# Performance work log

Measured on AMD Instinct MI355X. Metric: run time of the kernel, lower is better.

## Reference

```python
import jax, jax.numpy as jnp
import numpy as np

EPS_BN = 1e-3  # nn.BatchNorm1d(num_channels, eps=0.001)
B, C, N = 16, 256, 2048
NUM_SA = 4


def _bn(x, g, b, m, v):
    # eval-mode BatchNorm1d over channel dim of [B, C, N]
    return g[:, None] * (x - m[:, None]) * jax.lax.rsqrt(v[:, None] + EPS_BN) + b[:, None]


def _sa_layer(x, qk_w, v_w, v_b, t_w, t_b, g, b, m, var):
    # q_conv and k_conv share weights -> energy = (Wx)^T (Wx)
    q = jnp.einsum('oc,bcn->bon', qk_w, x)              # [B, C//4, N]
    energy = jnp.einsum('bcm,bcn->bmn', q, q)           # [B, N, N]
    attn = jax.nn.softmax(energy, axis=-1)
    # offset-attention: extra column-sum normalization (dim=1)
    attn = attn / (1e-9 + attn.sum(axis=1, keepdims=True))
    xv = jnp.einsum('oc,bcn->bon', v_w, x) + v_b[:, None]   # [B, C, N]
    x_r = jnp.einsum('bcn,bnm->bcm', xv, attn)              # bmm(x_v, attention)
    t = jnp.einsum('oc,bcn->bon', t_w, x - x_r) + t_b[:, None]
    return x + jax.nn.relu(_bn(t, g, b, m, var))


def setup_inputs() -> dict:
    key = jax.random.key(0)
    ks = jax.random.split(key, 24)
    f32 = jnp.float32
    d = {}
    d['x'] = jax.random.normal(ks[0], (B, C, N), dtype=f32)
    d['conv1_w'] = jax.random.normal(ks[1], (C, C), dtype=f32) * 0.05
    d['conv2_w'] = jax.random.normal(ks[2], (C, C), dtype=f32) * 0.05
    for i, nm in enumerate(['bn1', 'bn2']):
        kk = jax.random.split(ks[3 + i], 4)
        d[nm + '_g'] = 1.0 + 0.05 * jax.random.normal(kk[0], (C,), dtype=f32)
        d[nm + '_b'] = 0.05 * jax.random.normal(kk[1], (C,), dtype=f32)
        d[nm + '_m'] = 0.05 * jax.random.normal(kk[2], (C,), dtype=f32)
        d[nm + '_v'] = jax.random.uniform(kk[3], (C,), dtype=f32, minval=0.5, maxval=1.5)
    d['sa_qk_w'] = jax.random.normal(ks[5], (NUM_SA, C // 4, C), dtype=f32) * 0.05
    d['sa_v_w'] = jax.random.normal(ks[6], (NUM_SA, C, C), dtype=f32) * 0.05
    d['sa_v_b'] = jax.random.normal(ks[7], (NUM_SA, C), dtype=f32) * 0.05
    d['sa_t_w'] = jax.random.normal(ks[8], (NUM_SA, C, C), dtype=f32) * 0.05
    d['sa_t_b'] = jax.random.normal(ks[9], (NUM_SA, C), dtype=f32) * 0.05
    d['sa_g'] = 1.0 + 0.05 * jax.random.normal(ks[10], (NUM_SA, C), dtype=f32)
    d['sa_b'] = 0.05 * jax.random.normal(ks[11], (NUM_SA, C), dtype=f32)
    d['sa_m'] = 0.05 * jax.random.normal(ks[12], (NUM_SA, C), dtype=f32)
    d['sa_var'] = jax.random.uniform(ks[13], (NUM_SA, C), dtype=f32, minval=0.5, maxval=1.5)
    d['flag'] = 0  # False -> primary bn branch
    return d


def reference(x, conv1_w, conv2_w, bn1_g, bn1_b, bn1_m, bn1_v,
              bn2_g, bn2_b, bn2_m, bn2_v,
              sa_qk_w, sa_v_w, sa_v_b, sa_t_w, sa_t_b,
              sa_g, sa_b, sa_m, sa_var, flag):
    h = jax.nn.relu(_bn(jnp.einsum('oc,bcn->bon', conv1_w, x), bn1_g, bn1_b, bn1_m, bn1_v))
    h = jax.nn.relu(_bn(jnp.einsum('oc,bcn->bon', conv2_w, h), bn2_g, bn2_b, bn2_m, bn2_v))
    outs = []
    for i in range(NUM_SA):
        h = _sa_layer(h, sa_qk_w[i], sa_v_w[i], sa_v_b[i], sa_t_w[i], sa_t_b[i],
                      sa_g[i], sa_b[i], sa_m[i], sa_var[i])
        outs.append(h)
    return jnp.concatenate(outs, axis=1)  # [B, 4*C, N]
```

## Files before the change

### kernel.cpp

```cpp
#include <hip/hip_runtime.h>
#include <hip/hip_bf16.h>
#include <hip/hip_fp16.h>

static constexpr int Bn = 16;
static constexpr int Cc = 256;
static constexpr int Nn = 2048;
static constexpr int C4 = 64;
static constexpr float LOG2E = 1.4426950408889634f;

typedef _Float16 half_t;
typedef __attribute__((ext_vector_type(8))) _Float16 half8;
typedef __attribute__((ext_vector_type(4))) _Float16 half4;
typedef __attribute__((ext_vector_type(8))) short short8;
typedef __attribute__((ext_vector_type(4))) float float4v;

static constexpr long sNC = (long)Nn * Cc;
static constexpr long sNQ = (long)Nn * C4;

#define DEVI __device__ __forceinline__

DEVI float bf2f(unsigned short u) { return __uint_as_float(((unsigned)u) << 16); }
DEVI unsigned short f2bf(float f) {
    unsigned x = __float_as_uint(f);
    x += 0x7fffu + ((x >> 16) & 1u);
    return (unsigned short)(x >> 16);
}

DEVI void gload16(const void* g, void* l) {
    __builtin_amdgcn_global_load_lds(
        (const __attribute__((address_space(1))) unsigned int*)g,
        (__attribute__((address_space(3))) unsigned int*)l, 16, 0, 0);
}

enum { EPI_RAW = 0, EPI_H = 1, EPI_XV = 2, EPI_T = 4 };

template<int MODE, int BM, int BN, int WI, int WJ, bool BF16OUT>
__global__ __launch_bounds__(256)
void mgemm(const half_t* __restrict__ A, long aB,
           const half_t* __restrict__ Bm, long bB,
           void* __restrict__ Yv, long yB, int ldy,
           const half_t* __restrict__ Haux, long hB,
           half_t* __restrict__ hNext, long hnB,
           const float* __restrict__ bias,
           const float* __restrict__ bng, const float* __restrict__ bnb,
           const float* __restrict__ bnm, const float* __restrict__ bnv,
           int K)
{
    __shared__ __align__(16) half_t Als[2][BM][32];
    __shared__ __align__(16) half_t Bls[2][BN][32];

    const int tid  = threadIdx.x;
    const int w    = tid >> 6;
    const int lane = tid & 63;
    const int wi   = (WI == 1) ? 0 : (w & (WI - 1));
    const int wj   = (WI == 1) ? w : (w >> 1);
    const int quad = lane >> 4, m16 = lane & 15;
    const int lr   = lane >> 2, lc = lane & 3;
    const int b    = blockIdx.z;
    const int j0   = blockIdx.x * BN;
    const int i0   = blockIdx.y * BM;

    const half_t* Ab = A + (size_t)b * aB;
    const half_t* Bb = Bm + (size_t)b * bB;

    float4v acc[4][4];
    #pragma unroll
    for (int i = 0; i < 4; ++i)
        #pragma unroll
        for (int j = 0; j < 4; ++j) acc[i][j] = (float4v)0.f;

    for (int k0 = 0; k0 < K; k0 += 64) {
        #pragma unroll
        for (int s = 0; s < 2; ++s) {
            const int kk = k0 + s * 32 + lc * 8;
            #pragma unroll
            for (int t = 0; t < BM / 64; ++t) {
                const int row = (t * 4 + w) * 16;
                gload16(Ab + (size_t)(i0 + row + lr) * K + kk, &Als[s][row][0]);
            }
            #pragma unroll
            for (int t = 0; t < BN / 64; ++t) {
                const int row = (t * 4 + w) * 16;
                gload16(Bb + (size_t)(j0 + row + lr) * K + kk, &Bls[s][row][0]);
            }
        }
        __syncthreads();
        #pragma unroll
        for (int s = 0; s < 2; ++s) {
            half8 af[4], bf[4];
            #pragma unroll
            for (int t = 0; t < 4; ++t)
                af[t] = *(const half8*)&Als[s][wi * 64 + t * 16 + m16][quad * 8];
            #pragma unroll
            for (int t = 0; t < 4; ++t)
                bf[t] = *(const half8*)&Bls[s][wj * 64 + t * 16 + m16][quad * 8];
            #pragma unroll
            for (int ti = 0; ti < 4; ++ti)
                #pragma unroll
                for (int tj = 0; tj < 4; ++tj)
                    acc[ti][tj] = __builtin_amdgcn_mfma_f32_16x16x32_f16(
                        af[ti], bf[tj], acc[ti][tj], 0, 0, 0);
        }
        __syncthreads();
    }

    #pragma unroll
    for (int ti = 0; ti < 4; ++ti) {
        const int il = i0 + wi * 64 + ti * 16 + quad * 4;
        #pragma unroll
        for (int tj = 0; tj < 4; ++tj) {
            const int jl = j0 + wj * 64 + tj * 16 + m16;
            float4v v = acc[ti][tj];
            if (MODE == EPI_RAW) {
                half4 o;
                #pragma unroll
                for (int r = 0; r < 4; ++r) o[r] = (half_t)v[r];
                *(half4*)((half_t*)Yv + (size_t)b * yB + (size_t)jl * ldy + il) = o;
            } else if (MODE == EPI_H) {
                half4 o;
                #pragma unroll
                for (int r = 0; r < 4; ++r) {
                    const float sc = bng[il + r] * rsqrtf(bnv[il + r] + 1e-3f);
                    const float sh = bnb[il + r] - bnm[il + r] * sc;
                    o[r] = (half_t)fmaxf(fmaf(v[r], sc, sh), 0.f);
                }
                *(half4*)((half_t*)Yv + (size_t)b * yB + (size_t)jl * ldy + il) = o;
            } else if (MODE == EPI_XV) {
                const float bj = bias[jl];
                if (BF16OUT) {
                    ushort4 o;
                    o.x = f2bf(v[0] + bj); o.y = f2bf(v[1] + bj);
                    o.z = f2bf(v[2] + bj); o.w = f2bf(v[3] + bj);
                    *(ushort4*)((unsigned short*)Yv + (size_t)b * yB + (size_t)jl * ldy + il) = o;
                } else {
                    half4 o;
                    #pragma unroll
                    for (int r = 0; r < 4; ++r) o[r] = (half_t)(v[r] + bj);
                    *(half4*)((half_t*)Yv + (size_t)b * yB + (size_t)jl * ldy + il) = o;
                }
            } else {
                const float tb2 = bias[jl];
                const float sc  = bng[jl] * rsqrtf(bnv[jl] + 1e-3f);
                const float sh  = bnb[jl] - bnm[jl] * sc;
                float4v o;
                #pragma unroll
                for (int r = 0; r < 4; ++r) {
                    const float t2  = v[r] + tb2;
                    const float rel = fmaxf(fmaf(t2, sc, sh), 0.f);
                    const float hv  = (float)Haux[(size_t)b * hB + (size_t)(il + r) * Cc + jl];
                    const float ov  = hv + rel;
                    o[r] = ov;
                    if (hNext)
                        hNext[(size_t)b * hnB + (size_t)(il + r) * Cc + jl] = (half_t)ov;
                }
                *(float4v*)((float*)Yv + (size_t)b * yB + (size_t)jl * ldy + il) = o;
            }
        }
    }
}

__global__ __launch_bounds__(256)
void estats(const half_t* __restrict__ q, float* __restrict__ Pbuf)
{
    __shared__ __align__(16) half_t sA[128 * 64];
    __shared__ __align__(16) half_t sB[128 * 64];
    __shared__ float red[2][2][4][16][2];
    const int tid = threadIdx.x, w = tid >> 6, lane = tid & 63;
    const int wi = w & 1, wj = w >> 1, quad = lane >> 4, m16 = lane & 15;
    const int b = blockIdx.z, j0 = blockIdx.x * 128, i0 = blockIdx.y * 128;
    const half_t* qb = q + (size_t)b * sNQ;

    #pragma unroll
    for (int t = 0; t < 4; ++t) {
        const int g = w * 256 + t * 64 + lane;
        const int r = g >> 3, c = g & 7;
        const int cs = c ^ (r & 7);
        gload16(qb + (size_t)(i0 + r) * 64 + cs * 8, sA + (w * 256 + t * 64) * 8);
        gload16(qb + (size_t)(j0 + r) * 64 + cs * 8, sB + (w * 256 + t * 64) * 8);
    }
    __syncthreads();

    half8 an[4][2], bm[4][2];
    #pragma unroll
    for (int t = 0; t < 4; ++t)
        #pragma unroll
        for (int ks = 0; ks < 2; ++ks) {
            const int pc = ((ks * 4 + quad) ^ (m16 & 7)) * 8;
            an[t][ks] = *(const half8*)&sA[(wi * 64 + t * 16 + m16) * 64 + pc];
            bm[t][ks] = *(const half8*)&sB[(wj * 64 + t * 16 + m16) * 64 + pc];
        }

    #pragma unroll
    for (int tj = 0; tj < 4; ++tj) {
        float4v e[4];
        #pragma unroll
        for (int ti = 0; ti < 4; ++ti) {
            e[ti] = (float4v)0.f;
            e[ti] = __builtin_amdgcn_mfma_f32_16x16x32_f16(an[ti][0], bm[tj][0], e[ti], 0, 0, 0);
            e[ti] = __builtin_amdgcn_mfma_f32_16x16x32_f16(an[ti][1], bm[tj][1], e[ti], 0, 0, 0);
        }
        float lmax = -1e30f;
        #pragma unroll
        for (int ti = 0; ti < 4; ++ti)
            #pragma unroll
            for (int r = 0; r < 4; ++r) lmax = fmaxf(lmax, e[ti][r]);
        lmax = fmaxf(lmax, __shfl_xor(lmax, 16));
        lmax = fmaxf(lmax, __shfl_xor(lmax, 32));
        float ls = 0.f;
        #pragma unroll
        for (int ti = 0; ti < 4; ++ti)
            #pragma unroll
            for (int r = 0; r < 4; ++r) ls += __expf(e[ti][r] - lmax);
        ls += __shfl_xor(ls, 16);
        ls += __shfl_xor(ls, 32);
        if (quad == 0) { red[wi][wj][tj][m16][0] = lmax; red[wi][wj][tj][m16][1] = ls; }
    }
    __syncthreads();
    if (tid < 128) {
        const int wj2 = tid >> 6, tj2 = (tid >> 4) & 3, mm = tid & 15;
        const float m0 = red[0][wj2][tj2][mm][0], s0 = red[0][wj2][tj2][mm][1];
        const float m1 = red[1][wj2][tj2][mm][0], s1 = red[1][wj2][tj2][mm][1];
        const float M = fmaxf(m0, m1);
        const float S = s0 * __expf(m0 - M) + s1 * __expf(m1 - M);
        const int m = j0 + wj2 * 64 + tj2 * 16 + mm;
        *(float2*)(Pbuf + (((size_t)b * Nn + m) * 16 + blockIdx.y) * 2) = make_float2(M, S);
    }
}

__global__ __launch_bounds__(256)
void statsreduce(const float* __restrict__ Pbuf, float* __restrict__ off)
{
    const int id = blockIdx.x * 256 + threadIdx.x;
    const int b = id >> 11, m = id & 2047;
    const float2* p = (const float2*)(Pbuf + ((size_t)b * Nn + m) * 32);
    float M = -1e30f;
    #pragma unroll
    for (int i = 0; i < 16; ++i) M = fmaxf(M, p[i].x);
    float S = 0.f;
    #pragma unroll
    for (int i = 0; i < 16; ++i) S += p[i].y * __expf(p[i].x - M);
    off[(size_t)b * Nn + m] = fmaf(M, LOG2E, __log2f(S));
}

__global__ __launch_bounds__(512, 4)
void flashxr(const half_t* __restrict__ q, const half_t* __restrict__ xv,
             const half_t* __restrict__ h, const float* __restrict__ off,
             half_t* __restrict__ dS)
{
    __shared__ __align__(16) half_t sQ[128 * 64];
    __shared__ __align__(16) half_t sXV[128 * 128];
    __shared__ __align__(16) half_t sP[128 * 128];

    const int tid = threadIdx.x, w = tid >> 6, lane = tid & 63;
    const int wi = w & 1, wj = w >> 1, quad = lane >> 4, m16 = lane & 15;
    const int b = blockIdx.z, j0 = blockIdx.x * 128, i0 = blockIdx.y * 128;
    const half_t* qb  = q + (size_t)b * sNQ;
    const half_t* xvb = xv + (size_t)b * sNC;

    #pragma unroll
    for (int t = 0; t < 2; ++t) {
        const int g = w * 128 + t * 64 + lane;
        const int r = g >> 3, c = g & 7;
        gload16(qb + (size_t)(j0 + r) * 64 + (c ^ (r & 7)) * 8, sP + (w * 128 + t * 64) * 8);
    }
    __syncthreads();
    half8 bq[2][2];
    #pragma unroll
    for (int tj = 0; tj < 2; ++tj)
        #pragma unroll
        for (int ks = 0; ks < 2; ++ks)
            bq[tj][ks] = *(const half8*)&sP[(wj * 32 + tj * 16 + m16) * 64
                                            + (((ks * 4 + quad) ^ (m16 & 7)) * 8)];
    __syncthreads();

    float4v acc[4][2];
    #pragma unroll
    for (int i = 0; i < 4; ++i)
        #pragma unroll
        for (int j = 0; j < 2; ++j) acc[i][j] = (float4v)0.f;
    float csa[2] = {0.f, 0.f};

    const float* offb = off + (size_t)b * Nn;

    for (int nc = 0; nc < 16; ++nc) {
        #pragma unroll
        for (int t = 0; t < 2; ++t) {
            const int g = w * 128 + t * 64 + lane;
            const int r = g >> 3, c = g & 7;
            gload16(qb + (size_t)(nc * 128 + r) * 64 + (c ^ (r & 7)) * 8,
                    sQ + (w * 128 + t * 64) * 8);
        }
        #pragma unroll
        for (int t = 0; t < 4; ++t) {
            const int g = w * 256 + t * 64 + lane;
            const int r = g >> 4, c = g & 15;
            gload16(xvb + (size_t)(i0 + r) * Nn + nc * 128 + (c ^ (r & 15)) * 8,
                    sXV + (w * 256 + t * 64) * 8);
        }
        __syncthreads();

        const int nbase = nc * 128 + wi * 64 + quad * 4;
        #pragma unroll
        for (int ti = 0; ti < 4; ++ti) {
            const int arow = (wi * 64 + ti * 16 + m16) * 64;
            const half8 an0 = *(const half8*)&sQ[arow + ((quad ^ (m16 & 7)) * 8)];
            const half8 an1 = *(const half8*)&sQ[arow + (((4 + quad) ^ (m16 & 7)) * 8)];
            float4v e0 = (float4v)0.f, e1 = (float4v)0.f;
            e0 = __builtin_amdgcn_mfma_f32_16x16x32_f16(an0, bq[0][0], e0, 0, 0, 0);
            e1 = __builtin_amdgcn_mfma_f32_16x16x32_f16(an0, bq[1][0], e1, 0, 0, 0);
            e0 = __builtin_amdgcn_mfma_f32_16x16x32_f16(an1, bq[0][1], e0, 0, 0, 0);
            e1 = __builtin_amdgcn_mfma_f32_16x16x32_f16(an1, bq[1][1], e1, 0, 0, 0);
            const float4v o4 = *(const float4v*)&offb[nbase + ti * 16];
            const int pc = wi * 8 + ti * 2 + (quad >> 1);
            const int sub = (quad & 1) * 4;
            {
                float c0 = 0.f; ushort4 pk;
                #pragma unroll
                for (int r = 0; r < 4; ++r) {
                    const float p = __builtin_amdgcn_exp2f(fmaf(e0[r], LOG2E, -o4[r]));
                    c0 += p; (&pk.x)[r] = f2bf(p);
                }
                csa[0] += c0;
                const int mrow = wj * 32 + m16;
                *(ushort4*)&((unsigned short*)sP)[(size_t)mrow * 128 + (pc ^ m16) * 8 + sub] = pk;
            }
            {
                float c1 = 0.f; ushort4 pk;
                #pragma unroll
                for (int r = 0; r < 4; ++r) {
                    const float p = __builtin_amdgcn_exp2f(fmaf(e1[r], LOG2E, -o4[r]));
                    c1 += p; (&pk.x)[r] = f2bf(p);
                }
                csa[1] += c1;
                const int mrow = wj * 32 + 16 + m16;
                *(ushort4*)&((unsigned short*)sP)[(size_t)mrow * 128 + (pc ^ m16) * 8 + sub] = pk;
            }
        }
        __syncthreads();

        #pragma unroll
        for (int ks = 0; ks < 4; ++ks) {
            short8 xa[4], pb[2];
            #pragma unroll
            for (int ti = 0; ti < 4; ++ti)
                xa[ti] = *(const short8*)&sXV[(wi * 64 + ti * 16 + m16) * 128
                                              + (((ks * 4 + quad) ^ m16) * 8)];
            #pragma unroll
            for (int tj = 0; tj < 2; ++tj)
                pb[tj] = *(const short8*)&sP[(wj * 32 + tj * 16 + m16) * 128
                                             + (((ks * 4 + quad) ^ m16) * 8)];
            #pragma unroll
            for (int ti = 0; ti < 4; ++ti)
                #pragma unroll
                for (int tj = 0; tj < 2; ++tj)
                    acc[ti][tj] = __builtin_amdgcn_mfma_f32_16x16x32_bf16(
                        xa[ti], pb[tj], acc[ti][tj], 0, 0, 0);
        }
        __syncthreads();
    }

    #pragma unroll
    for (int tj = 0; tj < 2; ++tj) {
        csa[tj] += __shfl_xor(csa[tj], 16);
        csa[tj] += __shfl_xor(csa[tj], 32);
    }
    float* fb = (float*)sP;
    if (lane < 16) {
        #pragma unroll
        for (int tj = 0; tj < 2; ++tj)
            fb[wi * 128 + wj * 32 + tj * 16 + lane] = csa[tj];
    }
    __syncthreads();
    float csr[2];
    #pragma unroll
    for (int tj = 0; tj < 2; ++tj) {
        const float c0 = fb[0   + wj * 32 + tj * 16 + m16];
        const float c1 = fb[128 + wj * 32 + tj * 16 + m16];
        csr[tj] = 1.0f / (1e-9f + c0 + c1);
    }

    const half_t* hb = h + (size_t)b * sNC;
    half_t* db = dS + (size_t)b * sNC;
    #pragma unroll
    for (int ti = 0; ti < 4; ++ti) {
        const int cg = i0 + wi * 64 + ti * 16 + quad * 4;
        #pragma unroll
        for (int tj = 0; tj < 2; ++tj) {
            const int mg = j0 + wj * 32 + tj * 16 + m16;
            const half4 hv = *(const half4*)&hb[(size_t)mg * Cc + cg];
            half4 o;
            #pragma unroll
            for (int r = 0; r < 4; ++r)
                o[r] = (half_t)((float)hv[r] - acc[ti][tj][r] * csr[tj]);
            *(half4*)&db[(size_t)mg * Cc + cg] = o;
        }
    }
}

__global__ __launch_bounds__(256)
void xpose_cast(const float* __restrict__ x, half_t* __restrict__ xT)
{
    __shared__ half_t tile[32][33];
    const int tx = threadIdx.x & 31, ty = threadIdx.x >> 5;
    const int n0 = blockIdx.x * 32, c0 = blockIdx.y * 32, b = blockIdx.z;
    #pragma unroll
    for (int r = 0; r < 4; ++r)
        tile[ty * 4 + r][tx] =
            (half_t)x[((size_t)b * Cc + c0 + ty * 4 + r) * Nn + n0 + tx];
    __syncthreads();
    #pragma unroll
    for (int r = 0; r < 4; ++r)
        xT[((size_t)b * Nn + n0 + ty * 4 + r) * Cc + c0 + tx] = tile[tx][ty * 4 + r];
}

__global__ __launch_bounds__(256)
void castall(const float* __restrict__ c1, const float* __restrict__ c2,
             const float* __restrict__ qk, const float* __restrict__ vw,
             const float* __restrict__ tw, half_t* __restrict__ dst)
{
    const int i = (blockIdx.x * 256 + threadIdx.x) * 4;
    const float* s; int o;
    if      (i < 65536)  { s = c1; o = 0; }
    else if (i < 131072) { s = c2; o = 65536; }
    else if (i < 196608) { s = qk; o = 131072; }
    else if (i < 458752) { s = vw; o = 196608; }
    else                 { s = tw; o = 458752; }
    const float4v v = *(const float4v*)(s + (i - o));
    half4 out;
    #pragma unroll
    for (int r = 0; r < 4; ++r) out[r] = (half_t)v[r];
    *(half4*)(dst + i) = out;
}

extern "C" void kernel_launch(void* const* d_in, const int* in_sizes, int n_in,
                              void* d_out, int out_size, void* d_ws, size_t ws_size,
                              hipStream_t stream)
{
    const float* x    = (const float*)d_in[0];
    const float* c1w  = (const float*)d_in[1];
    const float* c2w  = (const float*)d_in[2];
    const float* bn1g = (const float*)d_in[3], *bn1b = (const float*)d_in[4];
    const float* bn1m = (const float*)d_in[5], *bn1v = (const float*)d_in[6];
    const float* bn2g = (const float*)d_in[7], *bn2b = (const float*)d_in[8];
    const float* bn2m = (const float*)d_in[9], *bn2v = (const float*)d_in[10];
    const float* qkw  = (const float*)d_in[11];
    const float* vw   = (const float*)d_in[12];
    const float* vb   = (const float*)d_in[13];
    const float* tw   = (const float*)d_in[14];
    const float* tb   = (const float*)d_in[15];
    const float* sag  = (const float*)d_in[16];
    const float* sab  = (const float*)d_in[17];
    const float* sam  = (const float*)d_in[18];
    const float* sav  = (const float*)d_in[19];
    float* out = (float*)d_out;

    char* ws = (char*)d_ws;
    const size_t HSZ = (size_t)Bn * Nn * Cc * 2;
    half_t* xT   = (half_t*)(ws);
    half_t* hA   = (half_t*)(ws + HSZ);
    half_t* hBuf = (half_t*)(ws + 2 * HSZ);
    half_t* q_s  = (half_t*)(ws + 3 * HSZ);
    half_t* xv_s = (half_t*)(ws + 3 * HSZ + (size_t)4194304);
    half_t* d_s  = (half_t*)(ws + 4 * HSZ + (size_t)4194304);
    float*  offp = (float*) (ws + 5 * HSZ + (size_t)4194304);
    float*  Pbuf = (float*) (ws + 5 * HSZ + (size_t)4325376);
    half_t* warena = (half_t*)(ws + 5 * HSZ + (size_t)8519680);
    half_t* wc1  = warena;
    half_t* wc2  = wc1 + 65536;
    half_t* wqk  = wc2 + 65536;
    half_t* wv   = wqk + 65536;
    half_t* wt   = wv  + 262144;

    dim3 blk(256);

    castall<<<768, blk, 0, stream>>>(c1w, c2w, qkw, vw, tw, warena);
    xpose_cast<<<dim3(Nn / 32, Cc / 32, Bn), blk, 0, stream>>>(x, xT);

    mgemm<EPI_H, 128, 128, 2, 2, false><<<dim3(16, 2, Bn), blk, 0, stream>>>(
        wc1, 0, xT, sNC, hA, sNC, Cc, nullptr, 0, nullptr, 0,
        nullptr, bn1g, bn1b, bn1m, bn1v, Cc);
    mgemm<EPI_H, 128, 128, 2, 2, false><<<dim3(16, 2, Bn), blk, 0, stream>>>(
        wc2, 0, hA, sNC, hBuf, sNC, Cc, nullptr, 0, nullptr, 0,
        nullptr, bn2g, bn2b, bn2m, bn2v, Cc);

    half_t* hcur = hBuf;
    half_t* hnxt = hA;
    for (int L = 0; L < 4; ++L) {
        mgemm<EPI_RAW, 64, 256, 1, 4, false><<<dim3(8, 1, Bn), blk, 0, stream>>>(
            wqk + (long)L * C4 * Cc, 0, hcur, sNC, q_s, sNQ, C4,
            nullptr, 0, nullptr, 0,
            nullptr, nullptr, nullptr, nullptr, nullptr, Cc);
        estats<<<dim3(16, 16, Bn), blk, 0, stream>>>(q_s, Pbuf);
        statsreduce<<<128, blk, 0, stream>>>(Pbuf, offp);
        mgemm<EPI_XV, 128, 128, 2, 2, true><<<dim3(2, 16, Bn), blk, 0, stream>>>(
            hcur, sNC, wv + (long)L * Cc * Cc, 0, xv_s, (long)Cc * Nn, Nn,
            nullptr, 0, nullptr, 0,
            vb + L * Cc, nullptr, nullptr, nullptr, nullptr, Cc);
        flashxr<<<dim3(16, 2, Bn), dim3(512), 0, stream>>>(
            q_s, xv_s, hcur, offp, d_s);
        mgemm<EPI_T, 128, 128, 2, 2, false><<<dim3(2, 16, Bn), blk, 0, stream>>>(
            d_s, sNC, wt + (long)L * Cc * Cc, 0,
            out + (long)L * Cc * Nn, (long)4 * Cc * Nn, Nn,
            hcur, sNC, (L < 3) ? hnxt : nullptr, sNC,
            tb + L * Cc, sag + L * Cc, sab + L * Cc, sam + L * Cc, sav + L * Cc,
            Cc);
        half_t* tmp = hcur; hcur = hnxt; hnxt = tmp;
    }
}
```

Baseline: 806.9 us.

## Widen flash kernel to full channel tile and enlarge GEMM blocks to 512 threads

```diff
diff --git a/kernel.cpp b/kernel.cpp
--- a/kernel.cpp
+++ b/kernel.cpp
@@ -35,7 +35,7 @@
 enum { EPI_RAW = 0, EPI_H = 1, EPI_XV = 2, EPI_T = 4 };
 
 template<int MODE, int BM, int BN, int WI, int WJ, bool BF16OUT>
-__global__ __launch_bounds__(256)
+__global__ __launch_bounds__(WI * WJ * 64)
 void mgemm(const half_t* __restrict__ A, long aB,
            const half_t* __restrict__ Bm, long bB,
            void* __restrict__ Yv, long yB, int ldy,
@@ -46,14 +46,15 @@
            const float* __restrict__ bnm, const float* __restrict__ bnv,
            int K)
 {
+    constexpr int NW = WI * WJ;
     __shared__ __align__(16) half_t Als[2][BM][32];
     __shared__ __align__(16) half_t Bls[2][BN][32];
 
     const int tid  = threadIdx.x;
     const int w    = tid >> 6;
     const int lane = tid & 63;
-    const int wi   = (WI == 1) ? 0 : (w & (WI - 1));
-    const int wj   = (WI == 1) ? w : (w >> 1);
+    const int wi   = w % WI;
+    const int wj   = w / WI;
     const int quad = lane >> 4, m16 = lane & 15;
     const int lr   = lane >> 2, lc = lane & 3;
     const int b    = blockIdx.z;
@@ -74,13 +75,13 @@
         for (int s = 0; s < 2; ++s) {
             const int kk = k0 + s * 32 + lc * 8;
             #pragma unroll
-            for (int t = 0; t < BM / 64; ++t) {
-                const int row = (t * 4 + w) * 16;
+            for (int t = 0; t < BM / (16 * NW); ++t) {
+                const int row = (t * NW + w) * 16;
                 gload16(Ab + (size_t)(i0 + row + lr) * K + kk, &Als[s][row][0]);
             }
             #pragma unroll
-            for (int t = 0; t < BN / 64; ++t) {
-                const int row = (t * 4 + w) * 16;
+            for (int t = 0; t < BN / (16 * NW); ++t) {
+                const int row = (t * NW + w) * 16;
                 gload16(Bb + (size_t)(j0 + row + lr) * K + kk, &Bls[s][row][0]);
             }
         }
@@ -242,35 +243,34 @@
     off[(size_t)b * Nn + m] = fmaf(M, LOG2E, __log2f(S));
 }
 
-__global__ __launch_bounds__(512, 4)
+__global__ __launch_bounds__(1024, 4)
 void flashxr(const half_t* __restrict__ q, const half_t* __restrict__ xv,
              const half_t* __restrict__ h, const float* __restrict__ off,
              half_t* __restrict__ dS)
 {
     __shared__ __align__(16) half_t sQ[128 * 64];
-    __shared__ __align__(16) half_t sXV[128 * 128];
+    __shared__ __align__(16) half_t sXV[256 * 128];
     __shared__ __align__(16) half_t sP[128 * 128];
 
     const int tid = threadIdx.x, w = tid >> 6, lane = tid & 63;
-    const int wi = w & 1, wj = w >> 1, quad = lane >> 4, m16 = lane & 15;
-    const int b = blockIdx.z, j0 = blockIdx.x * 128, i0 = blockIdx.y * 128;
+    const int quad = lane >> 4, m16 = lane & 15;
+    const int wiE = w & 1, wjE = w >> 1;
+    const int wi = w & 3, wj = w >> 2;
+    const int b = blockIdx.z, j0 = blockIdx.x * 128;
     const half_t* qb  = q + (size_t)b * sNQ;
     const half_t* xvb = xv + (size_t)b * sNC;
 
-    #pragma unroll
-    for (int t = 0; t < 2; ++t) {
-        const int g = w * 128 + t * 64 + lane;
-        const int r = g >> 3, c = g & 7;
-        gload16(qb + (size_t)(j0 + r) * 64 + (c ^ (r & 7)) * 8, sP + (w * 128 + t * 64) * 8);
-    }
-    __syncthreads();
-    half8 bq[2][2];
-    #pragma unroll
-    for (int tj = 0; tj < 2; ++tj)
-        #pragma unroll
-        for (int ks = 0; ks < 2; ++ks)
-            bq[tj][ks] = *(const half8*)&sP[(wj * 32 + tj * 16 + m16) * 64
-                                            + (((ks * 4 + quad) ^ (m16 & 7)) * 8)];
+    const int sr = tid >> 3, sc = tid & 7;
+    const int qsw = (sc ^ (sr & 7)) * 8;
+
+    gload16(qb + (size_t)(j0 + sr) * 64 + qsw, sP + (size_t)tid * 8);
+    gload16(qb + (size_t)sr * 64 + qsw,        sQ + (size_t)tid * 8);
+    __syncthreads();
+    half8 bq[2];
+    #pragma unroll
+    for (int ks = 0; ks < 2; ++ks)
+        bq[ks] = *(const half8*)&sP[(wjE * 16 + m16) * 64
+                                    + (((ks * 4 + quad) ^ (m16 & 7)) * 8)];
     __syncthreads();
 
     float4v acc[4][2];
@@ -278,65 +278,47 @@
     for (int i = 0; i < 4; ++i)
         #pragma unroll
         for (int j = 0; j < 2; ++j) acc[i][j] = (float4v)0.f;
-    float csa[2] = {0.f, 0.f};
+    float csa = 0.f;
 
     const float* offb = off + (size_t)b * Nn;
 
     for (int nc = 0; nc < 16; ++nc) {
         #pragma unroll
-        for (int t = 0; t < 2; ++t) {
-            const int g = w * 128 + t * 64 + lane;
-            const int r = g >> 3, c = g & 7;
-            gload16(qb + (size_t)(nc * 128 + r) * 64 + (c ^ (r & 7)) * 8,
-                    sQ + (w * 128 + t * 64) * 8);
-        }
-        #pragma unroll
         for (int t = 0; t < 4; ++t) {
-            const int g = w * 256 + t * 64 + lane;
+            const int g = t * 1024 + tid;
             const int r = g >> 4, c = g & 15;
-            gload16(xvb + (size_t)(i0 + r) * Nn + nc * 128 + (c ^ (r & 15)) * 8,
-                    sXV + (w * 256 + t * 64) * 8);
+            gload16(xvb + (size_t)r * Nn + nc * 128 + ((c ^ (r & 15)) * 8),
+                    sXV + (size_t)g * 8);
         }
         __syncthreads();
 
-        const int nbase = nc * 128 + wi * 64 + quad * 4;
+        const int nbase = nc * 128 + wiE * 64 + quad * 4;
         #pragma unroll
         for (int ti = 0; ti < 4; ++ti) {
-            const int arow = (wi * 64 + ti * 16 + m16) * 64;
+            const int arow = (wiE * 64 + ti * 16 + m16) * 64;
             const half8 an0 = *(const half8*)&sQ[arow + ((quad ^ (m16 & 7)) * 8)];
             const half8 an1 = *(const half8*)&sQ[arow + (((4 + quad) ^ (m16 & 7)) * 8)];
-            float4v e0 = (float4v)0.f, e1 = (float4v)0.f;
-            e0 = __builtin_amdgcn_mfma_f32_16x16x32_f16(an0, bq[0][0], e0, 0, 0, 0);
-            e1 = __builtin_amdgcn_mfma_f32_16x16x32_f16(an0, bq[1][0], e1, 0, 0, 0);
-            e0 = __builtin_amdgcn_mfma_f32_16x16x32_f16(an1, bq[0][1], e0, 0, 0, 0);
-            e1 = __builtin_amdgcn_mfma_f32_16x16x32_f16(an1, bq[1][1], e1, 0, 0, 0);
+            float4v e = (float4v)0.f;
+            e = __builtin_amdgcn_mfma_f32_16x16x32_f16(an0, bq[0], e, 0, 0, 0);
+            e = __builtin_amdgcn_mfma_f32_16x16x32_f16(an1, bq[1], e, 0, 0, 0);
             const float4v o4 = *(const float4v*)&offb[nbase + ti * 16];
-            const int pc = wi * 8 + ti * 2 + (quad >> 1);
+            float c0 = 0.f; ushort4 pk;
+            #pragma unroll
+            for (int r = 0; r < 4; ++r) {
+                const float p = __builtin_amdgcn_exp2f(fmaf(e[r], LOG2E, -o4[r]));
+                c0 += p; (&pk.x)[r] = f2bf(p);
+            }
+            csa += c0;
+            const int pc  = wiE * 8 + ti * 2 + (quad >> 1);
             const int sub = (quad & 1) * 4;
-            {
-                float c0 = 0.f; ushort4 pk;
-                #pragma unroll
-                for (int r = 0; r < 4; ++r) {
-                    const float p = __builtin_amdgcn_exp2f(fmaf(e0[r], LOG2E, -o4[r]));
-                    c0 += p; (&pk.x)[r] = f2bf(p);
-                }
-                csa[0] += c0;
-                const int mrow = wj * 32 + m16;
-                *(ushort4*)&((unsigned short*)sP)[(size_t)mrow * 128 + (pc ^ m16) * 8 + sub] = pk;
-            }
-            {
-                float c1 = 0.f; ushort4 pk;
-                #pragma unroll
-                for (int r = 0; r < 4; ++r) {
-                    const float p = __builtin_amdgcn_exp2f(fmaf(e1[r], LOG2E, -o4[r]));
-                    c1 += p; (&pk.x)[r] = f2bf(p);
-                }
-                csa[1] += c1;
-                const int mrow = wj * 32 + 16 + m16;
-                *(ushort4*)&((unsigned short*)sP)[(size_t)mrow * 128 + (pc ^ m16) * 8 + sub] = pk;
-            }
+            const int mrow = wjE * 16 + m16;
+            *(ushort4*)&((unsigned short*)sP)[(size_t)mrow * 128 + (pc ^ m16) * 8 + sub] = pk;
         }
         __syncthreads();
+
+        if (nc < 15)
+            gload16(qb + (size_t)((nc + 1) * 128 + sr) * 64 + qsw,
+                    sQ + (size_t)tid * 8);
 
         #pragma unroll
         for (int ks = 0; ks < 4; ++ks) {
@@ -359,31 +341,23 @@
         __syncthreads();
     }
 
+    csa += __shfl_xor(csa, 16);
+    csa += __shfl_xor(csa, 32);
+    float* fb = (float*)sP;
+    if (lane < 16) fb[wiE * 128 + wjE * 16 + lane] = csa;
+    __syncthreads();
+    float csr[2];
     #pragma unroll
     for (int tj = 0; tj < 2; ++tj) {
-        csa[tj] += __shfl_xor(csa[tj], 16);
-        csa[tj] += __shfl_xor(csa[tj], 32);
-    }
-    float* fb = (float*)sP;
-    if (lane < 16) {
-        #pragma unroll
-        for (int tj = 0; tj < 2; ++tj)
-            fb[wi * 128 + wj * 32 + tj * 16 + lane] = csa[tj];
-    }
-    __syncthreads();
-    float csr[2];
-    #pragma unroll
-    for (int tj = 0; tj < 2; ++tj) {
-        const float c0 = fb[0   + wj * 32 + tj * 16 + m16];
-        const float c1 = fb[128 + wj * 32 + tj * 16 + m16];
-        csr[tj] = 1.0f / (1e-9f + c0 + c1);
+        const int m = wj * 32 + tj * 16 + m16;
+        csr[tj] = 1.0f / (1e-9f + fb[m] + fb[128 + m]);
     }
 
     const half_t* hb = h + (size_t)b * sNC;
     half_t* db = dS + (size_t)b * sNC;
     #pragma unroll
     for (int ti = 0; ti < 4; ++ti) {
-        const int cg = i0 + wi * 64 + ti * 16 + quad * 4;
+        const int cg = wi * 64 + ti * 16 + quad * 4;
         #pragma unroll
         for (int tj = 0; tj < 2; ++tj) {
             const int mg = j0 + wj * 32 + tj * 16 + m16;
@@ -476,10 +450,10 @@
     castall<<<768, blk, 0, stream>>>(c1w, c2w, qkw, vw, tw, warena);
     xpose_cast<<<dim3(Nn / 32, Cc / 32, Bn), blk, 0, stream>>>(x, xT);
 
-    mgemm<EPI_H, 128, 128, 2, 2, false><<<dim3(16, 2, Bn), blk, 0, stream>>>(
+    mgemm<EPI_H, 256, 128, 4, 2, false><<<dim3(16, 1, Bn), dim3(512), 0, stream>>>(
         wc1, 0, xT, sNC, hA, sNC, Cc, nullptr, 0, nullptr, 0,
         nullptr, bn1g, bn1b, bn1m, bn1v, Cc);
-    mgemm<EPI_H, 128, 128, 2, 2, false><<<dim3(16, 2, Bn), blk, 0, stream>>>(
+    mgemm<EPI_H, 256, 128, 4, 2, false><<<dim3(16, 1, Bn), dim3(512), 0, stream>>>(
         wc2, 0, hA, sNC, hBuf, sNC, Cc, nullptr, 0, nullptr, 0,
         nullptr, bn2g, bn2b, bn2m, bn2v, Cc);
 
@@ -492,13 +466,13 @@
             nullptr, nullptr, nullptr, nullptr, nullptr, Cc);
         estats<<<dim3(16, 16, Bn), blk, 0, stream>>>(q_s, Pbuf);
         statsreduce<<<128, blk, 0, stream>>>(Pbuf, offp);
-        mgemm<EPI_XV, 128, 128, 2, 2, true><<<dim3(2, 16, Bn), blk, 0, stream>>>(
+        mgemm<EPI_XV, 128, 256, 2, 4, true><<<dim3(1, 16, Bn), dim3(512), 0, stream>>>(
             hcur, sNC, wv + (long)L * Cc * Cc, 0, xv_s, (long)Cc * Nn, Nn,
             nullptr, 0, nullptr, 0,
             vb + L * Cc, nullptr, nullptr, nullptr, nullptr, Cc);
-        flashxr<<<dim3(16, 2, Bn), dim3(512), 0, stream>>>(
+        flashxr<<<dim3(16, 1, Bn), dim3(1024), 0, stream>>>(
             q_s, xv_s, hcur, offp, d_s);
-        mgemm<EPI_T, 128, 128, 2, 2, false><<<dim3(2, 16, Bn), blk, 0, stream>>>(
+        mgemm<EPI_T, 128, 256, 2, 4, false><<<dim3(1, 16, Bn), dim3(512), 0, stream>>>(
             d_s, sNC, wt + (long)L * Cc * Cc, 0,
             out + (long)L * Cc * Nn, (long)4 * Cc * Nn, Nn,
             hcur, sNC, (L < 3) ? hnxt : nullptr, sNC,
```

New measurement: 795.7 us. Within noise of the previous version (-1.4%).
